# Optimization experiments

Hardware: AMD Instinct MI355X
Metric: run time of the kernel (lower is better)

Reference implementation:

```python
import jax, jax.numpy as jnp
import numpy as np

B, H, W, DIM = 8, 1024, 1024, 33


def setup_inputs() -> dict:
    key = jax.random.key(0)
    x = jax.random.uniform(key, (B, 3, H, W), dtype=jnp.float32)
    # Identity 3D LUT matching IdentityLUT{dim}.txt layout: n = i*D*D + j*D + k,
    # channel0 = k/(D-1) (red), channel1 = j/(D-1) (green), channel2 = i/(D-1) (blue).
    ax = jnp.arange(DIM, dtype=jnp.float32) / (DIM - 1)
    i, j, k = jnp.meshgrid(ax, ax, ax, indexing='ij')
    LUT = jnp.stack([k, j, i], axis=0)  # [3, D, D, D]
    return {"x": x, "LUT": LUT}


def _trilinear_lut(LUT, x):
    # LUT: [3, D, D, D] with spatial axes (i=depth, j=height, k=width).
    # x:   [B, 3, H, W] in [0,1]. grid_sample grid coord order is (w, h, d),
    # so red -> k axis, green -> j axis, blue -> i axis.
    D = LUT.shape[1]
    g = (x - 0.5) * 2.0                       # [-1, 1] grid (as in torch code)
    t = (g + 1.0) * 0.5 * (D - 1)             # align_corners=True unnormalize
    t = jnp.clip(t, 0.0, D - 1)               # padding_mode='border'
    r, gc, b = t[:, 0], t[:, 1], t[:, 2]      # each [B, H, W]

    def floor_ceil(c):
        f = jnp.floor(c)
        w = c - f
        f = f.astype(jnp.int32)
        return f, jnp.minimum(f + 1, D - 1), w

    k0, k1, wk = floor_ceil(r)
    j0, j1, wj = floor_ceil(gc)
    i0, i1, wi = floor_ceil(b)

    flat = LUT.reshape(3, -1)                 # [3, D^3]

    def gather(ii, jj, kk):
        idx = (ii * D + jj) * D + kk          # [B, H, W]
        return flat[:, idx]                   # [3, B, H, W]

    c00 = gather(i0, j0, k0) * (1 - wk) + gather(i0, j0, k1) * wk
    c01 = gather(i0, j1, k0) * (1 - wk) + gather(i0, j1, k1) * wk
    c10 = gather(i1, j0, k0) * (1 - wk) + gather(i1, j0, k1) * wk
    c11 = gather(i1, j1, k0) * (1 - wk) + gather(i1, j1, k1) * wk
    out = (c00 * (1 - wj) + c01 * wj) * (1 - wi) + (c10 * (1 - wj) + c11 * wj) * wi
    return jnp.transpose(out, (1, 0, 2, 3))   # [B, 3, H, W]


def reference(x, LUT):
    return _trilinear_lut(LUT, x)
```

## Files before the change

kernel.cpp:

```cpp
#include <hip/hip_runtime.h>
#include <hip/hip_fp16.h>

constexpr int D      = 33;
constexpr int LUTSZ  = D * D * D;
constexpr int PLANE  = 1024 * 1024;
constexpr int BATCH  = 8;
constexpr int NCELL  = 32 * 32 * 32;
constexpr size_t CELL_BYTES   = (size_t)NCELL * 64;
constexpr size_t PACKED_BYTES = (size_t)LUTSZ * 16;

typedef float        v4f __attribute__((ext_vector_type(4)));
typedef unsigned int v4u __attribute__((ext_vector_type(4)));

struct Rgb { float c0, c1, c2; };

__device__ __forceinline__ unsigned int pack_h2(float lo, float hi)
{
    __half2 h = __floats2half2_rn(lo, hi);
    return *reinterpret_cast<unsigned int*>(&h);
}

__device__ __forceinline__ float lerp_h2(unsigned int u, float w)
{
    __half2 h = *reinterpret_cast<__half2*>(&u);
    float lo = __half2float(__low2half(h));
    float hi = __half2float(__high2half(h));
    return fmaf(w, hi - lo, lo);
}

__global__ __launch_bounds__(256)
void pack_cells_kernel(const float* __restrict__ lut, v4u* __restrict__ T)
{
    int c = blockIdx.x * blockDim.x + threadIdx.x;
    if (c >= NCELL) return;
    int i0 = c >> 10, j0 = (c >> 5) & 31, k0 = c & 31;
    int base = (i0 * D + j0) * D + k0;

#pragma unroll
    for (int ch = 0; ch < 3; ++ch) {
        const float* __restrict__ L = lut + ch * LUTSZ;
        v4u e;
        e.x = pack_h2(L[base],             L[base + 1]);
        e.y = pack_h2(L[base + D],         L[base + D + 1]);
        e.z = pack_h2(L[base + D * D],     L[base + D * D + 1]);
        e.w = pack_h2(L[base + D * D + D], L[base + D * D + D + 1]);
        T[c * 4 + ch] = e;
    }
    T[c * 4 + 3] = (v4u)(0u);
}

__device__ __forceinline__ Rgb apply_lut_cell(const v4u* __restrict__ T,
                                              float r, float g, float b)
{
    float tr = fminf(fmaxf(r * 32.0f, 0.0f), 32.0f);
    float tg = fminf(fmaxf(g * 32.0f, 0.0f), 32.0f);
    float tb = fminf(fmaxf(b * 32.0f, 0.0f), 32.0f);

    int k0 = min((int)tr, 31); float wk = tr - (float)k0;
    int j0 = min((int)tg, 31); float wj = tg - (float)j0;
    int i0 = min((int)tb, 31); float wi = tb - (float)i0;

    int cell4 = (((i0 << 5) | j0) << 5 | k0) << 2;

    v4u e0 = T[cell4 + 0];
    v4u e1 = T[cell4 + 1];
    v4u e2 = T[cell4 + 2];

    Rgb o;
    {
        float c00 = lerp_h2(e0.x, wk), c01 = lerp_h2(e0.y, wk);
        float c10 = lerp_h2(e0.z, wk), c11 = lerp_h2(e0.w, wk);
        float c0 = fmaf(wj, c01 - c00, c00);
        float c1 = fmaf(wj, c11 - c10, c10);
        o.c0 = fmaf(wi, c1 - c0, c0);
    }
    {
        float c00 = lerp_h2(e1.x, wk), c01 = lerp_h2(e1.y, wk);
        float c10 = lerp_h2(e1.z, wk), c11 = lerp_h2(e1.w, wk);
        float c0 = fmaf(wj, c01 - c00, c00);
        float c1 = fmaf(wj, c11 - c10, c10);
        o.c1 = fmaf(wi, c1 - c0, c0);
    }
    {
        float c00 = lerp_h2(e2.x, wk), c01 = lerp_h2(e2.y, wk);
        float c10 = lerp_h2(e2.z, wk), c11 = lerp_h2(e2.w, wk);
        float c0 = fmaf(wj, c01 - c00, c00);
        float c1 = fmaf(wj, c11 - c10, c10);
        o.c2 = fmaf(wi, c1 - c0, c0);
    }
    return o;
}

__global__ __launch_bounds__(256)
void lut3d_cell_kernel(const float* __restrict__ x,
                       const v4u* __restrict__ T,
                       float* __restrict__ out)
{
    const int tid = blockIdx.x * blockDim.x + threadIdx.x;
    const int p0  = tid << 2;
    const int b   = p0 >> 20;
    const int q   = p0 & (PLANE - 1);
    const int base = b * 3 * PLANE + q;

    const v4f rv = __builtin_nontemporal_load(reinterpret_cast<const v4f*>(x + base));
    const v4f gv = __builtin_nontemporal_load(reinterpret_cast<const v4f*>(x + base + PLANE));
    const v4f bv = __builtin_nontemporal_load(reinterpret_cast<const v4f*>(x + base + 2 * PLANE));

    Rgb p0r = apply_lut_cell(T, rv.x, gv.x, bv.x);
    Rgb p1r = apply_lut_cell(T, rv.y, gv.y, bv.y);
    Rgb p2r = apply_lut_cell(T, rv.z, gv.z, bv.z);
    Rgb p3r = apply_lut_cell(T, rv.w, gv.w, bv.w);

    v4f o0 = { p0r.c0, p1r.c0, p2r.c0, p3r.c0 };
    v4f o1 = { p0r.c1, p1r.c1, p2r.c1, p3r.c1 };
    v4f o2 = { p0r.c2, p1r.c2, p2r.c2, p3r.c2 };

    __builtin_nontemporal_store(o0, reinterpret_cast<v4f*>(out + base));
    __builtin_nontemporal_store(o1, reinterpret_cast<v4f*>(out + base + PLANE));
    __builtin_nontemporal_store(o2, reinterpret_cast<v4f*>(out + base + 2 * PLANE));
}

__global__ __launch_bounds__(256)
void pack_lut_kernel(const float* __restrict__ lut, v4u* __restrict__ P)
{
    int idx = blockIdx.x * blockDim.x + threadIdx.x;
    if (idx >= LUTSZ) return;
    int k = idx % D;
    v4u e = (v4u)(0u);
    if (k < D - 1) {
        e.x = pack_h2(lut[0 * LUTSZ + idx], lut[0 * LUTSZ + idx + 1]);
        e.y = pack_h2(lut[1 * LUTSZ + idx], lut[1 * LUTSZ + idx + 1]);
        e.z = pack_h2(lut[2 * LUTSZ + idx], lut[2 * LUTSZ + idx + 1]);
    }
    P[idx] = e;
}

__device__ __forceinline__ Rgb apply_lut_packed(const v4u* __restrict__ P,
                                                float r, float g, float b)
{
    float tr = fminf(fmaxf(r * 32.0f, 0.0f), 32.0f);
    float tg = fminf(fmaxf(g * 32.0f, 0.0f), 32.0f);
    float tb = fminf(fmaxf(b * 32.0f, 0.0f), 32.0f);
    int k0 = min((int)tr, D - 2); float wk = tr - (float)k0;
    int j0 = (int)tg; float wj = tg - (float)j0; int j1 = min(j0 + 1, D - 1);
    int i0 = (int)tb; float wi = tb - (float)i0; int i1 = min(i0 + 1, D - 1);
    v4u e00 = P[(i0 * D + j0) * D + k0];
    v4u e01 = P[(i0 * D + j1) * D + k0];
    v4u e10 = P[(i1 * D + j0) * D + k0];
    v4u e11 = P[(i1 * D + j1) * D + k0];
    Rgb o;
    {
        float c00 = lerp_h2(e00.x, wk), c01 = lerp_h2(e01.x, wk);
        float c10 = lerp_h2(e10.x, wk), c11 = lerp_h2(e11.x, wk);
        float c0 = fmaf(wj, c01 - c00, c00), c1 = fmaf(wj, c11 - c10, c10);
        o.c0 = fmaf(wi, c1 - c0, c0);
    }
    {
        float c00 = lerp_h2(e00.y, wk), c01 = lerp_h2(e01.y, wk);
        float c10 = lerp_h2(e10.y, wk), c11 = lerp_h2(e11.y, wk);
        float c0 = fmaf(wj, c01 - c00, c00), c1 = fmaf(wj, c11 - c10, c10);
        o.c1 = fmaf(wi, c1 - c0, c0);
    }
    {
        float c00 = lerp_h2(e00.z, wk), c01 = lerp_h2(e01.z, wk);
        float c10 = lerp_h2(e10.z, wk), c11 = lerp_h2(e11.z, wk);
        float c0 = fmaf(wj, c01 - c00, c00), c1 = fmaf(wj, c11 - c10, c10);
        o.c2 = fmaf(wi, c1 - c0, c0);
    }
    return o;
}

__global__ __launch_bounds__(256)
void lut3d_packed_kernel(const float* __restrict__ x,
                         const v4u* __restrict__ P,
                         float* __restrict__ out)
{
    const int tid = blockIdx.x * blockDim.x + threadIdx.x;
    const int p0  = tid << 2;
    const int b   = p0 >> 20;
    const int q   = p0 & (PLANE - 1);
    const int base = b * 3 * PLANE + q;
    const v4f rv = __builtin_nontemporal_load(reinterpret_cast<const v4f*>(x + base));
    const v4f gv = __builtin_nontemporal_load(reinterpret_cast<const v4f*>(x + base + PLANE));
    const v4f bv = __builtin_nontemporal_load(reinterpret_cast<const v4f*>(x + base + 2 * PLANE));
    Rgb p0r = apply_lut_packed(P, rv.x, gv.x, bv.x);
    Rgb p1r = apply_lut_packed(P, rv.y, gv.y, bv.y);
    Rgb p2r = apply_lut_packed(P, rv.z, gv.z, bv.z);
    Rgb p3r = apply_lut_packed(P, rv.w, gv.w, bv.w);
    v4f o0 = { p0r.c0, p1r.c0, p2r.c0, p3r.c0 };
    v4f o1 = { p0r.c1, p1r.c1, p2r.c1, p3r.c1 };
    v4f o2 = { p0r.c2, p1r.c2, p2r.c2, p3r.c2 };
    __builtin_nontemporal_store(o0, reinterpret_cast<v4f*>(out + base));
    __builtin_nontemporal_store(o1, reinterpret_cast<v4f*>(out + base + PLANE));
    __builtin_nontemporal_store(o2, reinterpret_cast<v4f*>(out + base + 2 * PLANE));
}

extern "C" void kernel_launch(void* const* d_in, const int* in_sizes, int n_in,
                              void* d_out, int out_size, void* d_ws, size_t ws_size,
                              hipStream_t stream)
{
    const float* x   = (const float*)d_in[0];
    const float* lut = (const float*)d_in[1];
    float* out       = (float*)d_out;

    const int n_threads = (BATCH * PLANE) / 4;
    dim3 block(256);
    dim3 grid(n_threads / 256);

    if (ws_size >= CELL_BYTES) {
        v4u* T = (v4u*)d_ws;
        pack_cells_kernel<<<NCELL / 256, 256, 0, stream>>>(lut, T);
        lut3d_cell_kernel<<<grid, block, 0, stream>>>(x, T, out);
    } else if (ws_size >= PACKED_BYTES) {
        v4u* P = (v4u*)d_ws;
        pack_lut_kernel<<<(LUTSZ + 255) / 256, 256, 0, stream>>>(lut, P);
        lut3d_packed_kernel<<<grid, block, 0, stream>>>(x, P, out);
    }
}
```

Before: 231.3 us.

## Software-pipeline LUT kernel with grid-stride loop prefetching next pixel chunk

The main cell kernel now processes four chunks per thread in a grid-stride loop. It issues the next chunk's input loads before interpolating the current one, with a sched_barrier to keep that order, so input reads overlap LUT gathers and math. The pack kernel is split across channels on the y grid dimension and no longer writes the unused fourth v4u slot. The cost is fewer waves in flight and higher register pressure.

```diff
diff --git a/kernel.cpp b/kernel.cpp
--- a/kernel.cpp
+++ b/kernel.cpp
@@ -9,10 +9,13 @@
 constexpr size_t CELL_BYTES   = (size_t)NCELL * 64;
 constexpr size_t PACKED_BYTES = (size_t)LUTSZ * 16;
 
+constexpr int NITER = 4;
+
 typedef float        v4f __attribute__((ext_vector_type(4)));
 typedef unsigned int v4u __attribute__((ext_vector_type(4)));
 
-struct Rgb { float c0, c1, c2; };
+struct Rgb   { float c0, c1, c2; };
+struct CellW { int cell4; float wk, wj, wi; };
 
 __device__ __forceinline__ unsigned int pack_h2(float lo, float hi)
 {
@@ -31,62 +34,61 @@
 __global__ __launch_bounds__(256)
 void pack_cells_kernel(const float* __restrict__ lut, v4u* __restrict__ T)
 {
-    int c = blockIdx.x * blockDim.x + threadIdx.x;
-    if (c >= NCELL) return;
-    int i0 = c >> 10, j0 = (c >> 5) & 31, k0 = c & 31;
-    int base = (i0 * D + j0) * D + k0;
-
-#pragma unroll
-    for (int ch = 0; ch < 3; ++ch) {
-        const float* __restrict__ L = lut + ch * LUTSZ;
-        v4u e;
-        e.x = pack_h2(L[base],             L[base + 1]);
-        e.y = pack_h2(L[base + D],         L[base + D + 1]);
-        e.z = pack_h2(L[base + D * D],     L[base + D * D + 1]);
-        e.w = pack_h2(L[base + D * D + D], L[base + D * D + D + 1]);
-        T[c * 4 + ch] = e;
-    }
-    T[c * 4 + 3] = (v4u)(0u);
-}
-
-__device__ __forceinline__ Rgb apply_lut_cell(const v4u* __restrict__ T,
-                                              float r, float g, float b)
+    const int cell = blockIdx.x * blockDim.x + threadIdx.x;
+    const int ch   = blockIdx.y;
+    if (cell >= NCELL) return;
+    const int i0 = cell >> 10, j0 = (cell >> 5) & 31, k0 = cell & 31;
+    const int base = (i0 * D + j0) * D + k0;
+
+    const float* __restrict__ L = lut + ch * LUTSZ;
+    v4u e;
+    e.x = pack_h2(L[base],             L[base + 1]);
+    e.y = pack_h2(L[base + D],         L[base + D + 1]);
+    e.z = pack_h2(L[base + D * D],     L[base + D * D + 1]);
+    e.w = pack_h2(L[base + D * D + D], L[base + D * D + D + 1]);
+    T[cell * 4 + ch] = e;
+}
+
+__device__ __forceinline__ CellW cell_of(float r, float g, float b)
 {
     float tr = fminf(fmaxf(r * 32.0f, 0.0f), 32.0f);
     float tg = fminf(fmaxf(g * 32.0f, 0.0f), 32.0f);
     float tb = fminf(fmaxf(b * 32.0f, 0.0f), 32.0f);
 
-    int k0 = min((int)tr, 31); float wk = tr - (float)k0;
-    int j0 = min((int)tg, 31); float wj = tg - (float)j0;
-    int i0 = min((int)tb, 31); float wi = tb - (float)i0;
-
-    int cell4 = (((i0 << 5) | j0) << 5 | k0) << 2;
-
-    v4u e0 = T[cell4 + 0];
-    v4u e1 = T[cell4 + 1];
-    v4u e2 = T[cell4 + 2];
-
+    int k0 = min((int)tr, 31);
+    int j0 = min((int)tg, 31);
+    int i0 = min((int)tb, 31);
+    CellW w;
+    w.wk = tr - (float)k0;
+    w.wj = tg - (float)j0;
+    w.wi = tb - (float)i0;
+    w.cell4 = (((i0 << 5) | j0) << 5 | k0) << 2;
+    return w;
+}
+
+__device__ __forceinline__ Rgb lerp_cell(v4u e0, v4u e1, v4u e2, CellW w)
+{
     Rgb o;
     {
-        float c00 = lerp_h2(e0.x, wk), c01 = lerp_h2(e0.y, wk);
-        float c10 = lerp_h2(e0.z, wk), c11 = lerp_h2(e0.w, wk);
-        float c0 = fmaf(wj, c01 - c00, c00);
-        float c1 = fmaf(wj, c11 - c10, c10);
-        o.c0 = fmaf(wi, c1 - c0, c0);
-    }
-    {
-        float c00 = lerp_h2(e1.x, wk), c01 = lerp_h2(e1.y, wk);
-        float c10 = lerp_h2(e1.z, wk), c11 = lerp_h2(e1.w, wk);
-        float c0 = fmaf(wj, c01 - c00, c00);
-        float c1 = fmaf(wj, c11 - c10, c10);
-        o.c1 = fmaf(wi, c1 - c0, c0);
-    }
-    {
-        float c00 = lerp_h2(e2.x, wk), c01 = lerp_h2(e2.y, wk);
-        float c10 = lerp_h2(e2.z, wk), c11 = lerp_h2(e2.w, wk);
-        float c0 = fmaf(wj, c01 - c00, c00);
-        float c1 = fmaf(wj, c11 - c10, c10);
-        o.c2 = fmaf(wi, c1 - c0, c0);
+        float c00 = lerp_h2(e0.x, w.wk), c01 = lerp_h2(e0.y, w.wk);
+        float c10 = lerp_h2(e0.z, w.wk), c11 = lerp_h2(e0.w, w.wk);
+        float c0 = fmaf(w.wj, c01 - c00, c00);
+        float c1 = fmaf(w.wj, c11 - c10, c10);
+        o.c0 = fmaf(w.wi, c1 - c0, c0);
+    }
+    {
+        float c00 = lerp_h2(e1.x, w.wk), c01 = lerp_h2(e1.y, w.wk);
+        float c10 = lerp_h2(e1.z, w.wk), c11 = lerp_h2(e1.w, w.wk);
+        float c0 = fmaf(w.wj, c01 - c00, c00);
+        float c1 = fmaf(w.wj, c11 - c10, c10);
+        o.c1 = fmaf(w.wi, c1 - c0, c0);
+    }
+    {
+        float c00 = lerp_h2(e2.x, w.wk), c01 = lerp_h2(e2.y, w.wk);
+        float c10 = lerp_h2(e2.z, w.wk), c11 = lerp_h2(e2.w, w.wk);
+        float c0 = fmaf(w.wj, c01 - c00, c00);
+        float c1 = fmaf(w.wj, c11 - c10, c10);
+        o.c2 = fmaf(w.wi, c1 - c0, c0);
     }
     return o;
 }
@@ -96,28 +98,66 @@
                        const v4u* __restrict__ T,
                        float* __restrict__ out)
 {
-    const int tid = blockIdx.x * blockDim.x + threadIdx.x;
-    const int p0  = tid << 2;
-    const int b   = p0 >> 20;
-    const int q   = p0 & (PLANE - 1);
-    const int base = b * 3 * PLANE + q;
-
-    const v4f rv = __builtin_nontemporal_load(reinterpret_cast<const v4f*>(x + base));
-    const v4f gv = __builtin_nontemporal_load(reinterpret_cast<const v4f*>(x + base + PLANE));
-    const v4f bv = __builtin_nontemporal_load(reinterpret_cast<const v4f*>(x + base + 2 * PLANE));
-
-    Rgb p0r = apply_lut_cell(T, rv.x, gv.x, bv.x);
-    Rgb p1r = apply_lut_cell(T, rv.y, gv.y, bv.y);
-    Rgb p2r = apply_lut_cell(T, rv.z, gv.z, bv.z);
-    Rgb p3r = apply_lut_cell(T, rv.w, gv.w, bv.w);
-
-    v4f o0 = { p0r.c0, p1r.c0, p2r.c0, p3r.c0 };
-    v4f o1 = { p0r.c1, p1r.c1, p2r.c1, p3r.c1 };
-    v4f o2 = { p0r.c2, p1r.c2, p2r.c2, p3r.c2 };
-
-    __builtin_nontemporal_store(o0, reinterpret_cast<v4f*>(out + base));
-    __builtin_nontemporal_store(o1, reinterpret_cast<v4f*>(out + base + PLANE));
-    __builtin_nontemporal_store(o2, reinterpret_cast<v4f*>(out + base + 2 * PLANE));
+    const int tid    = blockIdx.x * blockDim.x + threadIdx.x;
+    const int stride = gridDim.x * blockDim.x;
+
+    int c = tid;
+    int base;
+    v4f rv, gv, bv;
+    {
+        const int p0 = c << 2;
+        const int b  = p0 >> 20;
+        const int q  = p0 & (PLANE - 1);
+        base = b * 3 * PLANE + q;
+        rv = __builtin_nontemporal_load(reinterpret_cast<const v4f*>(x + base));
+        gv = __builtin_nontemporal_load(reinterpret_cast<const v4f*>(x + base + PLANE));
+        bv = __builtin_nontemporal_load(reinterpret_cast<const v4f*>(x + base + 2 * PLANE));
+    }
+
+#pragma unroll
+    for (int it = 0; it < NITER; ++it) {
+        const CellW w0 = cell_of(rv.x, gv.x, bv.x);
+        const CellW w1 = cell_of(rv.y, gv.y, bv.y);
+        const CellW w2 = cell_of(rv.z, gv.z, bv.z);
+        const CellW w3 = cell_of(rv.w, gv.w, bv.w);
+
+        const v4u* __restrict__ t0 = T + w0.cell4;
+        const v4u* __restrict__ t1 = T + w1.cell4;
+        const v4u* __restrict__ t2 = T + w2.cell4;
+        const v4u* __restrict__ t3 = T + w3.cell4;
+        const v4u e00 = t0[0], e01 = t0[1], e02 = t0[2];
+        const v4u e10 = t1[0], e11 = t1[1], e12 = t1[2];
+        const v4u e20 = t2[0], e21 = t2[1], e22 = t2[2];
+        const v4u e30 = t3[0], e31 = t3[1], e32 = t3[2];
+
+        const int cn = c + stride;
+        int basen = base;
+        v4f rn = rv, gn = gv, bn = bv;
+        if (it + 1 < NITER) {
+            const int p0 = cn << 2;
+            const int b  = p0 >> 20;
+            const int q  = p0 & (PLANE - 1);
+            basen = b * 3 * PLANE + q;
+            rn = __builtin_nontemporal_load(reinterpret_cast<const v4f*>(x + basen));
+            gn = __builtin_nontemporal_load(reinterpret_cast<const v4f*>(x + basen + PLANE));
+            bn = __builtin_nontemporal_load(reinterpret_cast<const v4f*>(x + basen + 2 * PLANE));
+        }
+        __builtin_amdgcn_sched_barrier(0);
+
+        const Rgb q0 = lerp_cell(e00, e01, e02, w0);
+        const Rgb q1 = lerp_cell(e10, e11, e12, w1);
+        const Rgb q2 = lerp_cell(e20, e21, e22, w2);
+        const Rgb q3 = lerp_cell(e30, e31, e32, w3);
+
+        v4f o0 = { q0.c0, q1.c0, q2.c0, q3.c0 };
+        v4f o1 = { q0.c1, q1.c1, q2.c1, q3.c1 };
+        v4f o2 = { q0.c2, q1.c2, q2.c2, q3.c2 };
+        __builtin_nontemporal_store(o0, reinterpret_cast<v4f*>(out + base));
+        __builtin_nontemporal_store(o1, reinterpret_cast<v4f*>(out + base + PLANE));
+        __builtin_nontemporal_store(o2, reinterpret_cast<v4f*>(out + base + 2 * PLANE));
+
+        rv = rn; gv = gn; bv = bn; base = basen; c = cn;
+    }
 }
 
 __global__ __launch_bounds__(256)
@@ -203,17 +243,16 @@
     const float* lut = (const float*)d_in[1];
     float* out       = (float*)d_out;
 
-    const int n_threads = (BATCH * PLANE) / 4;
-    dim3 block(256);
-    dim3 grid(n_threads / 256);
-
     if (ws_size >= CELL_BYTES) {
         v4u* T = (v4u*)d_ws;
-        pack_cells_kernel<<<NCELL / 256, 256, 0, stream>>>(lut, T);
-        lut3d_cell_kernel<<<grid, block, 0, stream>>>(x, T, out);
+        pack_cells_kernel<<<dim3(NCELL / 256, 3), 256, 0, stream>>>(lut, T);
+        const int n_chunks  = (BATCH * PLANE) / 4;
+        const int n_threads = n_chunks / NITER;
+        lut3d_cell_kernel<<<n_threads / 256, 256, 0, stream>>>(x, T, out);
     } else if (ws_size >= PACKED_BYTES) {
         v4u* P = (v4u*)d_ws;
         pack_lut_kernel<<<(LUTSZ + 255) / 256, 256, 0, stream>>>(lut, P);
-        lut3d_packed_kernel<<<grid, block, 0, stream>>>(x, P, out);
-    }
-}
+        const int n_threads = (BATCH * PLANE) / 4;
+        lut3d_packed_kernel<<<n_threads / 256, 256, 0, stream>>>(x, P, out);
+    }
+}
```

Measured after the change: 222.8 us. -3.7%, faster.
